# Performance work log

Hardware: AMD Instinct MI355X
Metric: run time of the kernel (lower is better)

## Reference

```python
import jax, jax.numpy as jnp
import numpy as np

EMB = 1024
HEADS = 8
EXP = 4
EPS = 1e-5


def setup_inputs() -> dict:
    key = jax.random.key(0)
    ks = jax.random.split(key, 12)
    s = 0.02
    return {
        "x": jax.random.normal(ks[0], (4, 2048, EMB), dtype=jnp.float32),
        "wqkv_w": jax.random.normal(ks[1], (EMB, 3 * EMB), dtype=jnp.float32) * s,
        "wqkv_b": jnp.zeros((3 * EMB,), dtype=jnp.float32),
        "proj_w": jax.random.normal(ks[2], (EMB, EMB), dtype=jnp.float32) * s,
        "proj_b": jnp.zeros((EMB,), dtype=jnp.float32),
        "lin1_w": jax.random.normal(ks[3], (EMB, EXP * EMB), dtype=jnp.float32) * s,
        "lin1_b": jnp.zeros((EXP * EMB,), dtype=jnp.float32),
        "lin2_w": jax.random.normal(ks[4], (EXP * EMB, EMB), dtype=jnp.float32) * s,
        "lin2_b": jnp.zeros((EMB,), dtype=jnp.float32),
        "ln_g": jnp.ones((EMB,), dtype=jnp.float32),
        "ln_b": jnp.zeros((EMB,), dtype=jnp.float32),
    }


def _layernorm(x, g, b):
    mu = jnp.mean(x, axis=-1, keepdims=True)
    var = jnp.var(x, axis=-1, keepdims=True)
    return (x - mu) * jax.lax.rsqrt(var + EPS) * g + b


def reference(x, wqkv_w, wqkv_b, proj_w, proj_b, lin1_w, lin1_b, lin2_w, lin2_b, ln_g, ln_b):
    b, n, e = x.shape
    h = HEADS
    d = e // h
    # fused QKV; source splits '(h d w)' with w=3 innermost (interleaved)
    w = x @ wqkv_w + wqkv_b                      # [b, n, 3e]
    w = w.reshape(b, n, h, d, 3)
    w = jnp.transpose(w, (4, 0, 2, 1, 3))        # [3, b, h, n, d]
    q, k, v = w[0], w[1], w[2]
    scores = jnp.einsum('bhqd,bhkd->bhqk', q, k)  # unscaled logits (as in source)
    attn = jax.nn.softmax(scores, axis=-1) / jnp.sqrt(jnp.float32(e))
    o = jnp.einsum('bhqk,bhkd->bhqd', attn, v)
    o = jnp.transpose(o, (0, 2, 1, 3)).reshape(b, n, e)
    mha = o @ proj_w + proj_b
    x = _layernorm(x + mha, ln_g, ln_b)
    ff = (jax.nn.gelu(x @ lin1_w + lin1_b, approximate=False)) @ lin2_w + lin2_b
    return _layernorm(x + ff, ln_g, ln_b)
```

## Files before the change

kernel.cpp:

```cpp
#include <hip/hip_runtime.h>
#include <hip/hip_bf16.h>
#include <math.h>

#define B_DIM 4
#define SEQ   2048
#define EMB   1024
#define HEADS 8
#define DHEAD 128
#define M_TOK (B_DIM * SEQ)
#define FFDIM (4 * EMB)

typedef unsigned short u16;
typedef __attribute__((ext_vector_type(8))) short short8v;
typedef __attribute__((ext_vector_type(4))) float float4v;
typedef __attribute__((ext_vector_type(16))) float float16v;

__device__ __forceinline__ u16 f2b(float f) {
  union { float f; unsigned u; } a; a.f = f;
  unsigned u = a.u;
  u += 0x7fffu + ((u >> 16) & 1u);
  return (u16)(u >> 16);
}

__device__ __forceinline__ u16 f2b_hw(float f) {
  __hip_bfloat16 h = __float2bfloat16(f);
  return *(u16*)&h;
}

__device__ __forceinline__ void gload16(const void* g, void* l) {
  __builtin_amdgcn_global_load_lds(
      (const __attribute__((address_space(1))) unsigned int*)g,
      (__attribute__((address_space(3))) unsigned int*)l, 16, 0, 0);
}

__device__ __forceinline__ float gelu_inl(float v) {
  const float y = 0.7978845608028654f * (v + 0.044715f * v * v * v);
  const float e = __expf(2.0f * y);
  const float th = 1.0f - 2.0f / (e + 1.0f);
  return 0.5f * v * (1.0f + th);
}

__device__ __forceinline__ void tcvt_body(const float* __restrict__ W,
    u16* __restrict__ Wt, int K, int N, int bx, int by, int tx, int ty,
    float (*t)[33]) {
  const int n0 = bx * 32, k0 = by * 32;
  for (int j = ty; j < 32; j += 8)
    t[j][tx] = W[(size_t)(k0 + j) * N + n0 + tx];
  __syncthreads();
  for (int j = ty; j < 32; j += 8)
    Wt[(size_t)(n0 + j) * K + k0 + tx] = f2b(t[tx][j]);
}

__global__ __launch_bounds__(256) void k_prep(
    const float* __restrict__ x, const float* __restrict__ wqkv_w,
    const float* __restrict__ proj_w, const float* __restrict__ lin1_w,
    const float* __restrict__ lin2_w, u16* __restrict__ xb,
    u16* __restrict__ wqkv_t, u16* __restrict__ proj_t,
    u16* __restrict__ lin1_t, u16* __restrict__ lin2_t) {
  __shared__ float t[32][33];
  const int bid = blockIdx.x, tid = threadIdx.x;
  if (bid < 8192) {
    const int i = bid * 256 + tid;
    const float4 v = ((const float4*)x)[i];
    unsigned long long pk = (unsigned long long)f2b(v.x)
        | ((unsigned long long)f2b(v.y) << 16)
        | ((unsigned long long)f2b(v.z) << 32)
        | ((unsigned long long)f2b(v.w) << 48);
    ((unsigned long long*)xb)[i] = pk;
    return;
  }
  const int tx = tid & 31, ty = tid >> 5;
  if (bid < 11264)
    tcvt_body(wqkv_w, wqkv_t, 1024, 3072, (bid - 8192) % 96, (bid - 8192) / 96, tx, ty, t);
  else if (bid < 12288)
    tcvt_body(proj_w, proj_t, 1024, 1024, (bid - 11264) % 32, (bid - 11264) / 32, tx, ty, t);
  else if (bid < 16384)
    tcvt_body(lin1_w, lin1_t, 1024, 4096, (bid - 12288) % 128, (bid - 12288) / 128, tx, ty, t);
  else
    tcvt_body(lin2_w, lin2_t, 4096, 1024, (bid - 16384) % 32, (bid - 16384) / 32, tx, ty, t);
}

template <int EPI>
__global__ __launch_bounds__(256, 2) void k_gemm(
    const u16* __restrict__ A, const u16* __restrict__ Bt,
    const float* __restrict__ bias, const float* __restrict__ res,
    void* __restrict__ out0, int M, int N, int K) {
  __shared__ __align__(16) u16 lds[2][2][128][32];
  const int tid = threadIdx.x;
  const int l = tid & 63, w = tid >> 6;
  const int g = l >> 4, lm = l & 15;
  const int wm = w >> 1, wn = w & 1;

  const int NBX = N >> 7;
  const int nwg = NBX * (M >> 7);
  const int wg = blockIdx.x;
  const int swz = (wg & 7) * (nwg >> 3) + (wg >> 3);
  const int tn = swz % NBX, tm = swz / NBX;

  const size_t arow0 = (size_t)tm * 128;
  const size_t brow0 = (size_t)tn * 128;
  const int srow = l >> 2;
  const int scol = (l & 3) * 8;

  float4v acc[4][4];
  const float4v vzero = {0.f, 0.f, 0.f, 0.f};
#pragma unroll
  for (int i = 0; i < 4; ++i)
#pragma unroll
    for (int j = 0; j < 4; ++j) acc[i][j] = vzero;

  const int nt = K / 32;
  auto stage = [&](int t, int buf) {
    const int k0 = t * 32;
#pragma unroll
    for (int i = 0; i < 2; ++i) {
      const int r = w * 32 + i * 16 + srow;
      gload16(A + (arow0 + r) * (size_t)K + k0 + scol, &lds[buf][0][w * 32 + i * 16][0]);
      gload16(Bt + (brow0 + r) * (size_t)K + k0 + scol, &lds[buf][1][w * 32 + i * 16][0]);
    }
  };

  stage(0, 0);
  __syncthreads();
  for (int t = 0; t < nt; ++t) {
    const int buf = t & 1;
    if (t + 1 < nt) stage(t + 1, buf ^ 1);
    short8v af[4], bf[4];
#pragma unroll
    for (int mf = 0; mf < 4; ++mf)
      af[mf] = *(const short8v*)&lds[buf][0][wm * 64 + mf * 16 + lm][g * 8];
#pragma unroll
    for (int nf = 0; nf < 4; ++nf)
      bf[nf] = *(const short8v*)&lds[buf][1][wn * 64 + nf * 16 + lm][g * 8];
#pragma unroll
    for (int mf = 0; mf < 4; ++mf)
#pragma unroll
      for (int nf = 0; nf < 4; ++nf)
        acc[mf][nf] = __builtin_amdgcn_mfma_f32_16x16x32_bf16(af[mf], bf[nf], acc[mf][nf], 0, 0, 0);
    __syncthreads();
  }

#pragma unroll
  for (int mf = 0; mf < 4; ++mf)
#pragma unroll
    for (int nf = 0; nf < 4; ++nf)
#pragma unroll
      for (int r = 0; r < 4; ++r) {
        const int row = tm * 128 + wm * 64 + mf * 16 + 4 * g + r;
        const int col = tn * 128 + wn * 64 + nf * 16 + lm;
        float v = acc[mf][nf][r] + bias[col];
        if constexpr (EPI == 0) {
          const int hh = col / 384;
          const int rem = col - hh * 384;
          const int d = rem / 3;
          const int wv = rem - d * 3;
          const int btok = row >> 11, ntok = row & 2047;
          u16* dst = (u16*)out0 + (size_t)wv * ((size_t)M_TOK * EMB)
                   + (((size_t)(btok * HEADS + hh) * SEQ + ntok) * DHEAD + d);
          *dst = f2b(v);
        } else if constexpr (EPI == 2) {
          ((u16*)out0)[(size_t)row * N + col] = f2b(gelu_inl(v));
        } else {
          const size_t idx = (size_t)row * N + col;
          ((float*)out0)[idx] = v + res[idx];
        }
      }
}

__global__ __launch_bounds__(256, 2) void k_attn(
    const u16* __restrict__ q, const u16* __restrict__ k,
    const u16* __restrict__ v, u16* __restrict__ o) {
  __shared__ __align__(16) u16 KT[2][64 * 128];
  __shared__ __align__(16) u16 VT[2][64 * 128];
  const int tid = threadIdx.x;
  const int l = tid & 63, w = tid >> 6;
  const int q32 = l & 31, hi = l >> 5;
  const int i = blockIdx.x;
  const int xcd = i & 7, j = i >> 3;
  const int bh = xcd * 4 + (j >> 4);
  const int qt = j & 15;
  const int hh = bh & 7, bb = bh >> 3;
  const size_t base = (size_t)(bb * HEADS + hh) * SEQ * DHEAD;
  const int qrow0 = qt * 128 + w * 32;

  short8v qf[8];
#pragma unroll
  for (int c = 0; c < 8; ++c)
    qf[c] = *(const short8v*)(q + base + (size_t)(qrow0 + q32) * DHEAD + c * 16 + hi * 8);

  float m = -1e30f, Sden = 0.f;
  float16v O[4];
#pragma unroll
  for (int nf = 0; nf < 4; ++nf)
#pragma unroll
    for (int r = 0; r < 16; ++r) O[nf][r] = 0.f;

  const int krow = tid >> 4;
  const int kseg = (tid & 15) * 16;
  const int vp = tid & 31, vdg = tid >> 5;

  short8v va_a, vb_a, va_b, vb_b;
  auto loadV = [&](int t) {
    const u16* s0p = v + base + ((size_t)t * 64 + 2 * vp) * DHEAD + vdg * 8;
    va_a = *(const short8v*)s0p;
    vb_a = *(const short8v*)(s0p + DHEAD);
    va_b = *(const short8v*)(s0p + 64);
    vb_b = *(const short8v*)(s0p + DHEAD + 64);
  };
  auto writeV = [&](int b) {
#pragma unroll
    for (int jj = 0; jj < 8; ++jj) {
      const int da = vdg * 8 + jj;
      const unsigned pka = ((unsigned)(u16)va_a[jj]) | (((unsigned)(u16)vb_a[jj]) << 16);
      const int bya = (da * 128 + 4 * vp) ^ ((da & 7) << 4);
      *(unsigned*)((char*)&VT[b][0] + bya) = pka;
      const int db = (vdg + 8) * 8 + jj;
      const unsigned pkb = ((unsigned)(u16)va_b[jj]) | (((unsigned)(u16)vb_b[jj]) << 16);
      const int byb = (db * 128 + 4 * vp) ^ ((db & 7) << 4);
      *(unsigned*)((char*)&VT[b][0] + byb) = pkb;
    }
  };
  auto stageK = [&](int t, int b) {
    const size_t kvbase = base + (size_t)t * 64 * DHEAD;
#pragma unroll
    for (int s = 0; s < 4; ++s) {
      const int r = s * 16 + krow;
      const int csrc = kseg ^ ((r & 7) << 4);
      gload16(k + kvbase + (size_t)r * DHEAD + (csrc >> 1),
              (u16*)&KT[b][0] + s * 2048 + tid * 8);
    }
  };

  loadV(0);
  stageK(0, 0);
  writeV(0);
  __syncthreads();

  for (int t = 0; t < 32; ++t) {
    const int buf = t & 1;
    const char* KTb = (const char*)&KT[buf][0];
    const char* VTb = (const char*)&VT[buf][0];
    if (t + 1 < 32) { loadV(t + 1); stageK(t + 1, buf ^ 1); }

    float16v S0, S1;
#pragma unroll
    for (int r = 0; r < 16; ++r) { S0[r] = 0.f; S1[r] = 0.f; }
    __builtin_amdgcn_s_setprio(1);
#pragma unroll
    for (int c = 0; c < 8; ++c) {
      const int cb = (c * 32 + hi * 16) ^ ((q32 & 7) << 4);
      const short8v kf0 = *(const short8v*)(KTb + q32 * 256 + cb);
      const short8v kf1 = *(const short8v*)(KTb + (32 + q32) * 256 + cb);
      S0 = __builtin_amdgcn_mfma_f32_32x32x16_bf16(kf0, qf[c], S0, 0, 0, 0);
      S1 = __builtin_amdgcn_mfma_f32_32x32x16_bf16(kf1, qf[c], S1, 0, 0, 0);
    }
    __builtin_amdgcn_s_setprio(0);

    float pm = -1e30f;
#pragma unroll
    for (int r = 0; r < 16; ++r) pm = fmaxf(pm, fmaxf(S0[r], S1[r]));
    pm = fmaxf(pm, __shfl_xor(pm, 32));
    if (!__all(pm <= m + 8.0f)) {
      const float nm = fmaxf(m, pm);
      const float rsc = __expf(m - nm);
      m = nm;
      Sden *= rsc;
#pragma unroll
      for (int r = 0; r < 16; ++r) {
        const float rr_ = __shfl(rsc, (r & 3) + 8 * (r >> 2) + 4 * hi, 64);
#pragma unroll
        for (int nf = 0; nf < 4; ++nf) O[nf][r] *= rr_;
      }
    }
    float ps = 0.f;
#pragma unroll
    for (int r = 0; r < 16; ++r) { S0[r] = __expf(S0[r] - m); ps += S0[r]; }
#pragma unroll
    for (int r = 0; r < 16; ++r) { S1[r] = __expf(S1[r] - m); ps += S1[r]; }
    ps += __shfl_xor(ps, 32);
    Sden += ps;

    unsigned u0[8], u1[8];
#pragma unroll
    for (int jj = 0; jj < 8; ++jj) {
      u0[jj] = (unsigned)f2b_hw(S0[2 * jj]) | ((unsigned)f2b_hw(S0[2 * jj + 1]) << 16);
      u1[jj] = (unsigned)f2b_hw(S1[2 * jj]) | ((unsigned)f2b_hw(S1[2 * jj + 1]) << 16);
    }

#pragma unroll
    for (int ks = 0; ks < 4; ++ks) {
      const int k1 = ks & 1;
      unsigned b0v, b1v, b2v, b3v;
      if (ks < 2) { b0v = u0[4 * k1]; b1v = u0[4 * k1 + 1]; b2v = u0[4 * k1 + 2]; b3v = u0[4 * k1 + 3]; }
      else        { b0v = u1[4 * k1]; b1v = u1[4 * k1 + 1]; b2v = u1[4 * k1 + 2]; b3v = u1[4 * k1 + 3]; }
      const unsigned send0 = hi ? b0v : b2v;
      const unsigned send1 = hi ? b1v : b3v;
      const unsigned rx0 = (unsigned)__shfl_xor((int)send0, 32);
      const unsigned rx1 = (unsigned)__shfl_xor((int)send1, 32);
      union { unsigned uu[4]; short8v s8; } pu;
      pu.uu[0] = hi ? rx0 : b0v;
      pu.uu[1] = hi ? rx1 : b1v;
      pu.uu[2] = hi ? b2v : rx0;
      pu.uu[3] = hi ? b3v : rx1;
      __builtin_amdgcn_s_setprio(1);
#pragma unroll
      for (int nf = 0; nf < 4; ++nf) {
        const int dr = nf * 32 + q32;
        const int vb = (dr * 128 + ks * 32 + hi * 16) ^ ((dr & 7) << 4);
        const short8v vf = *(const short8v*)(VTb + vb);
        O[nf] = __builtin_amdgcn_mfma_f32_32x32x16_bf16(pu.s8, vf, O[nf], 0, 0, 0);
      }
      __builtin_amdgcn_s_setprio(0);
    }

    if (t + 1 < 32) writeV(buf ^ 1);
    __syncthreads();
  }

  const float si = 1.0f / (Sden * 32.0f);
#pragma unroll
  for (int r = 0; r < 16; ++r) {
    const int cr = (r & 3) + 8 * (r >> 2) + 4 * hi;
    const float sio = __shfl(si, cr, 64);
    const int tok = qrow0 + cr;
#pragma unroll
    for (int nf = 0; nf < 4; ++nf)
      o[(size_t)(bb * SEQ + tok) * EMB + hh * DHEAD + nf * 32 + q32] = f2b_hw(O[nf][r] * sio);
  }
}

template <int MODE>
__global__ __launch_bounds__(256) void k_ln(const float* __restrict__ in,
    const float* __restrict__ gw, const float* __restrict__ bw,
    float* __restrict__ outf, u16* __restrict__ outb) {
  __shared__ float ps[4], pq[4];
  const int row = blockIdx.x;
  const int t = threadIdx.x;
  const float4 v = ((const float4*)(in + (size_t)row * EMB))[t];
  float s = v.x + v.y + v.z + v.w;
  float sq = v.x * v.x + v.y * v.y + v.z * v.z + v.w * v.w;
#pragma unroll
  for (int d = 1; d < 64; d <<= 1) { s += __shfl_xor(s, d); sq += __shfl_xor(sq, d); }
  const int l = t & 63, w = t >> 6;
  if (l == 0) { ps[w] = s; pq[w] = sq; }
  __syncthreads();
  s = ps[0] + ps[1] + ps[2] + ps[3];
  sq = pq[0] + pq[1] + pq[2] + pq[3];
  const float mean = s * (1.0f / 1024.0f);
  const float var = sq * (1.0f / 1024.0f) - mean * mean;
  const float rs = rsqrtf(var + 1e-5f);
  const float4 gv = ((const float4*)gw)[t];
  const float4 bv = ((const float4*)bw)[t];
  float4 ov;
  ov.x = (v.x - mean) * rs * gv.x + bv.x;
  ov.y = (v.y - mean) * rs * gv.y + bv.y;
  ov.z = (v.z - mean) * rs * gv.z + bv.z;
  ov.w = (v.w - mean) * rs * gv.w + bv.w;
  ((float4*)(outf + (size_t)row * EMB))[t] = ov;
  if constexpr (MODE == 0) {
    unsigned long long pk = (unsigned long long)f2b(ov.x)
        | ((unsigned long long)f2b(ov.y) << 16)
        | ((unsigned long long)f2b(ov.z) << 32)
        | ((unsigned long long)f2b(ov.w) << 48);
    ((unsigned long long*)(outb + (size_t)row * EMB))[t] = pk;
  }
}

extern "C" void kernel_launch(void* const* d_in, const int* in_sizes, int n_in,
                              void* d_out, int out_size, void* d_ws, size_t ws_size,
                              hipStream_t stream) {
  const float* x      = (const float*)d_in[0];
  const float* wqkv_w = (const float*)d_in[1];
  const float* wqkv_b = (const float*)d_in[2];
  const float* proj_w = (const float*)d_in[3];
  const float* proj_b = (const float*)d_in[4];
  const float* lin1_w = (const float*)d_in[5];
  const float* lin1_b = (const float*)d_in[6];
  const float* lin2_w = (const float*)d_in[7];
  const float* lin2_b = (const float*)d_in[8];
  const float* ln_g   = (const float*)d_in[9];
  const float* ln_b   = (const float*)d_in[10];

  char* ws = (char*)d_ws;
  u16*   wqkv_t = (u16*)(ws + 0);
  u16*   proj_t = (u16*)(ws + 6291456);
  u16*   lin1_t = (u16*)(ws + 8388608);
  u16*   lin2_t = (u16*)(ws + 16777216);
  u16*   qbuf   = (u16*)(ws + 25165824);
  u16*   kbuf   = (u16*)(ws + 25165824 + 16777216);
  u16*   vbuf   = (u16*)(ws + 25165824 + 33554432);
  u16*   xb     = (u16*)(ws + 75497472);
  u16*   attn_o = (u16*)(ws + 75497472);
  float* res1   = (float*)(ws + 92274688);
  u16*   hbuf   = (u16*)(ws + 92274688);
  float* x1f    = (float*)(ws + 25165824);
  u16*   x1b    = (u16*)(ws + 58720256);
  float* outf   = (float*)d_out;

  k_prep<<<20480, 256, 0, stream>>>(x, wqkv_w, proj_w, lin1_w, lin2_w,
                                    xb, wqkv_t, proj_t, lin1_t, lin2_t);

  k_gemm<0><<<(3 * EMB / 128) * (M_TOK / 128), 256, 0, stream>>>(
      xb, wqkv_t, wqkv_b, nullptr, (void*)qbuf, M_TOK, 3 * EMB, EMB);
  k_attn<<<512, 256, 0, stream>>>(qbuf, kbuf, vbuf, attn_o);
  k_gemm<1><<<(EMB / 128) * (M_TOK / 128), 256, 0, stream>>>(
      attn_o, proj_t, proj_b, x, (void*)res1, M_TOK, EMB, EMB);
  k_ln<0><<<M_TOK, 256, 0, stream>>>(res1, ln_g, ln_b, x1f, x1b);
  k_gemm<2><<<(FFDIM / 128) * (M_TOK / 128), 256, 0, stream>>>(
      x1b, lin1_t, lin1_b, nullptr, (void*)hbuf, M_TOK, FFDIM, EMB);
  k_gemm<3><<<(EMB / 128) * (M_TOK / 128), 256, 0, stream>>>(
      hbuf, lin2_t, lin2_b, x1f, (void*)outf, M_TOK, EMB, FFDIM);
  k_ln<1><<<M_TOK, 256, 0, stream>>>(outf, ln_g, ln_b, outf, nullptr);
}
```

Before: 454.9 us.

## Rewrite GEMM as 8-wave 256-row tiles with 4-slot pipelined swizzled LDS

Result: no change. 463.9 us (+2.0%).

```diff
diff --git a/kernel.cpp b/kernel.cpp
--- a/kernel.cpp
+++ b/kernel.cpp
@@ -80,74 +80,146 @@
     tcvt_body(lin2_w, lin2_t, 4096, 1024, (bid - 16384) % 32, (bid - 16384) / 32, tx, ty, t);
 }
 
-template <int EPI>
-__global__ __launch_bounds__(256, 2) void k_gemm(
+template <int EPI, int BN>
+__global__ __launch_bounds__(512, 2) void k_gemm8(
     const u16* __restrict__ A, const u16* __restrict__ Bt,
     const float* __restrict__ bias, const float* __restrict__ res,
     void* __restrict__ out0, int M, int N, int K) {
-  __shared__ __align__(16) u16 lds[2][2][128][32];
+  constexpr int BM = 256, BK = 32;
+  constexpr int ASZ = BM * BK;
+  constexpr int BSZ = BN * BK;
+  constexpr int NLB = (BN == 256) ? 2 : 1;
+  constexpr int LPT = 2 + NLB;
+  constexpr int WN = BN / 4;
+  constexpr int NF = WN / 16;
+  __shared__ __align__(16) u16 LA[4][ASZ];
+  __shared__ __align__(16) u16 LB[4][BSZ];
+
   const int tid = threadIdx.x;
   const int l = tid & 63, w = tid >> 6;
   const int g = l >> 4, lm = l & 15;
-  const int wm = w >> 1, wn = w & 1;
-
-  const int NBX = N >> 7;
-  const int nwg = NBX * (M >> 7);
+  const int wm = w >> 2, wn = w & 3;
+
+  const int NBX = N / BN;
+  const int nwg = NBX * (M >> 8);
   const int wg = blockIdx.x;
   const int swz = (wg & 7) * (nwg >> 3) + (wg >> 3);
   const int tn = swz % NBX, tm = swz / NBX;
-
-  const size_t arow0 = (size_t)tm * 128;
-  const size_t brow0 = (size_t)tn * 128;
-  const int srow = l >> 2;
-  const int scol = (l & 3) * 8;
-
-  float4v acc[4][4];
+  const size_t arow0 = (size_t)tm * BM;
+  const size_t brow0 = (size_t)tn * BN;
+
+  float4v acc[8][NF];
   const float4v vzero = {0.f, 0.f, 0.f, 0.f};
 #pragma unroll
-  for (int i = 0; i < 4; ++i)
-#pragma unroll
-    for (int j = 0; j < 4; ++j) acc[i][j] = vzero;
-
-  const int nt = K / 32;
-  auto stage = [&](int t, int buf) {
-    const int k0 = t * 32;
+  for (int i = 0; i < 8; ++i)
+#pragma unroll
+    for (int j = 0; j < NF; ++j) acc[i][j] = vzero;
+
+  const int nt = K / BK;
+
+  auto stageA = [&](int t) {
+    const int slot = t & 3;
+    const int k0 = t * BK;
 #pragma unroll
     for (int i = 0; i < 2; ++i) {
-      const int r = w * 32 + i * 16 + srow;
-      gload16(A + (arow0 + r) * (size_t)K + k0 + scol, &lds[buf][0][w * 32 + i * 16][0]);
-      gload16(Bt + (brow0 + r) * (size_t)K + k0 + scol, &lds[buf][1][w * 32 + i * 16][0]);
-    }
-  };
-
-  stage(0, 0);
-  __syncthreads();
+      const int D = i * 8192 + tid * 16;
+      const int U = D ^ (((D >> 9) & 1) << 5);
+      const int rr = U >> 6;
+      const int cc = (U & 63) >> 1;
+      gload16(A + (arow0 + rr) * (size_t)K + k0 + cc,
+              (u16*)&LA[slot][0] + i * 4096 + w * 512);
+    }
+  };
+  auto stageB = [&](int t) {
+    const int slot = t & 3;
+    const int k0 = t * BK;
+#pragma unroll
+    for (int i = 0; i < NLB; ++i) {
+      const int D = i * 8192 + tid * 16;
+      const int U = D ^ (((D >> 9) & 1) << 5);
+      const int rr = U >> 6;
+      const int cc = (U & 63) >> 1;
+      gload16(Bt + (brow0 + rr) * (size_t)K + k0 + cc,
+              (u16*)&LB[slot][0] + i * 4096 + w * 512);
+    }
+  };
+  auto rdA = [&](int slot, int mf) -> short8v {
+    const int Lb = (wm * 128 + mf * 16 + lm) * 64 + g * 16;
+    const int Sb = Lb ^ (((Lb >> 9) & 1) << 5);
+    return *(const short8v*)((const char*)&LA[slot][0] + Sb);
+  };
+  auto rdB = [&](int slot, int nf) -> short8v {
+    const int Lb = (wn * WN + nf * 16 + lm) * 64 + g * 16;
+    const int Sb = Lb ^ (((Lb >> 9) & 1) << 5);
+    return *(const short8v*)((const char*)&LB[slot][0] + Sb);
+  };
+
+  stageA(0); stageB(0);
+  stageA(1); stageB(1);
+  if constexpr (BN == 256) asm volatile("s_waitcnt vmcnt(4)" ::: "memory");
+  else                     asm volatile("s_waitcnt vmcnt(3)" ::: "memory");
+  __builtin_amdgcn_s_barrier();
+
   for (int t = 0; t < nt; ++t) {
-    const int buf = t & 1;
-    if (t + 1 < nt) stage(t + 1, buf ^ 1);
-    short8v af[4], bf[4];
-#pragma unroll
-    for (int mf = 0; mf < 4; ++mf)
-      af[mf] = *(const short8v*)&lds[buf][0][wm * 64 + mf * 16 + lm][g * 8];
-#pragma unroll
-    for (int nf = 0; nf < 4; ++nf)
-      bf[nf] = *(const short8v*)&lds[buf][1][wn * 64 + nf * 16 + lm][g * 8];
-#pragma unroll
-    for (int mf = 0; mf < 4; ++mf)
-#pragma unroll
-      for (int nf = 0; nf < 4; ++nf)
-        acc[mf][nf] = __builtin_amdgcn_mfma_f32_16x16x32_bf16(af[mf], bf[nf], acc[mf][nf], 0, 0, 0);
-    __syncthreads();
+    const int slot = t & 3;
+    short8v a0 = rdA(slot, 0), a1 = rdA(slot, 1), a2 = rdA(slot, 2),
+            a3 = rdA(slot, 3), a4 = rdA(slot, 4), a5 = rdA(slot, 5),
+            a6 = rdA(slot, 6), a7 = rdA(slot, 7);
+    short8v b0 = rdB(slot, 0), b1 = rdB(slot, 1);
+    if (t + 2 < nt) {
+      stageA(t + 2);
+      if constexpr (NF == 2) stageB(t + 2);
+    }
+    __builtin_amdgcn_s_barrier();
+    asm volatile("s_waitcnt lgkmcnt(0)" ::: "memory");
+    __builtin_amdgcn_sched_barrier(0);
+    __builtin_amdgcn_s_setprio(1);
+#pragma unroll
+    for (int mf = 0; mf < 8; ++mf) {
+      const short8v am = (mf == 0) ? a0 : (mf == 1) ? a1 : (mf == 2) ? a2 :
+                         (mf == 3) ? a3 : (mf == 4) ? a4 : (mf == 5) ? a5 :
+                         (mf == 6) ? a6 : a7;
+      acc[mf][0] = __builtin_amdgcn_mfma_f32_16x16x32_bf16(am, b0, acc[mf][0], 0, 0, 0);
+      acc[mf][1] = __builtin_amdgcn_mfma_f32_16x16x32_bf16(am, b1, acc[mf][1], 0, 0, 0);
+    }
+    __builtin_amdgcn_s_setprio(0);
+    if constexpr (NF == 4) {
+      __builtin_amdgcn_s_barrier();
+      short8v b2 = rdB(slot, 2), b3 = rdB(slot, 3);
+      if (t + 2 < nt) stageB(t + 2);
+      __builtin_amdgcn_s_barrier();
+      asm volatile("s_waitcnt lgkmcnt(0)" ::: "memory");
+      __builtin_amdgcn_sched_barrier(0);
+      __builtin_amdgcn_s_setprio(1);
+#pragma unroll
+      for (int mf = 0; mf < 8; ++mf) {
+        const short8v am = (mf == 0) ? a0 : (mf == 1) ? a1 : (mf == 2) ? a2 :
+                           (mf == 3) ? a3 : (mf == 4) ? a4 : (mf == 5) ? a5 :
+                           (mf == 6) ? a6 : a7;
+        acc[mf][2] = __builtin_amdgcn_mfma_f32_16x16x32_bf16(am, b2, acc[mf][2], 0, 0, 0);
+        acc[mf][3] = __builtin_amdgcn_mfma_f32_16x16x32_bf16(am, b3, acc[mf][3], 0, 0, 0);
+      }
+      __builtin_amdgcn_s_setprio(0);
+    }
+    if (t + 1 < nt) {
+      if (t + 2 < nt) {
+        if constexpr (BN == 256) asm volatile("s_waitcnt vmcnt(4)" ::: "memory");
+        else                     asm volatile("s_waitcnt vmcnt(3)" ::: "memory");
+      } else {
+        asm volatile("s_waitcnt vmcnt(0)" ::: "memory");
+      }
+      __builtin_amdgcn_s_barrier();
+    }
   }
 
 #pragma unroll
-  for (int mf = 0; mf < 4; ++mf)
-#pragma unroll
-    for (int nf = 0; nf < 4; ++nf)
+  for (int mf = 0; mf < 8; ++mf)
+#pragma unroll
+    for (int nf = 0; nf < NF; ++nf)
 #pragma unroll
       for (int r = 0; r < 4; ++r) {
-        const int row = tm * 128 + wm * 64 + mf * 16 + 4 * g + r;
-        const int col = tn * 128 + wn * 64 + nf * 16 + lm;
+        const int row = tm * BM + wm * 128 + mf * 16 + 4 * g + r;
+        const int col = tn * BN + wn * WN + nf * 16 + lm;
         float v = acc[mf][nf][r] + bias[col];
         if constexpr (EPI == 0) {
           const int hh = col / 384;
@@ -400,15 +472,15 @@
   k_prep<<<20480, 256, 0, stream>>>(x, wqkv_w, proj_w, lin1_w, lin2_w,
                                     xb, wqkv_t, proj_t, lin1_t, lin2_t);
 
-  k_gemm<0><<<(3 * EMB / 128) * (M_TOK / 128), 256, 0, stream>>>(
+  k_gemm8<0, 256><<<(3 * EMB / 256) * (M_TOK / 256), 512, 0, stream>>>(
       xb, wqkv_t, wqkv_b, nullptr, (void*)qbuf, M_TOK, 3 * EMB, EMB);
   k_attn<<<512, 256, 0, stream>>>(qbuf, kbuf, vbuf, attn_o);
-  k_gemm<1><<<(EMB / 128) * (M_TOK / 128), 256, 0, stream>>>(
+  k_gemm8<1, 128><<<(EMB / 128) * (M_TOK / 256), 512, 0, stream>>>(
       attn_o, proj_t, proj_b, x, (void*)res1, M_TOK, EMB, EMB);
   k_ln<0><<<M_TOK, 256, 0, stream>>>(res1, ln_g, ln_b, x1f, x1b);
-  k_gemm<2><<<(FFDIM / 128) * (M_TOK / 128), 256, 0, stream>>>(
+  k_gemm8<2, 256><<<(FFDIM / 256) * (M_TOK / 256), 512, 0, stream>>>(
       x1b, lin1_t, lin1_b, nullptr, (void*)hbuf, M_TOK, FFDIM, EMB);
-  k_gemm<3><<<(EMB / 128) * (M_TOK / 128), 256, 0, stream>>>(
+  k_gemm8<3, 128><<<(EMB / 128) * (M_TOK / 256), 512, 0, stream>>>(
       hbuf, lin2_t, lin2_b, x1f, (void*)outf, M_TOK, EMB, FFDIM);
   k_ln<1><<<M_TOK, 256, 0, stream>>>(outf, ln_g, ln_b, outf, nullptr);
 }
```
